# Kernel tuning notes

Measured on AMD Instinct MI355X. Metric: run time of the kernel, lower is better.

The kernel has to match this reference:

```python
import jax, jax.numpy as jnp
import numpy as np

B, T, D = 2, 2048, 2048
H, HKV, HD = 16, 4, 128
I = 5632
EPS = 1e-5


def setup_inputs() -> dict:
    ks = jax.random.split(jax.random.key(0), 12)
    s = 0.02
    return {
        "x": jax.random.normal(ks[0], (B, T, D), jnp.float32),
        "rope_cos": jax.random.uniform(ks[1], (T, HD // 2), jnp.float32),
        "rope_sin": jax.random.uniform(ks[2], (T, HD // 2), jnp.float32),
        "ln1_w": jnp.ones((D,), jnp.float32),
        "ln2_w": jnp.ones((D,), jnp.float32),
        "wq_w": jax.random.normal(ks[3], (D, H * HD), jnp.float32) * s,
        "wq_b": jnp.zeros((H * HD,), jnp.float32),
        "wk_w": jax.random.normal(ks[4], (D, HKV * HD), jnp.float32) * s,
        "wk_b": jnp.zeros((HKV * HD,), jnp.float32),
        "wv_w": jax.random.normal(ks[5], (D, HKV * HD), jnp.float32) * s,
        "wv_b": jnp.zeros((HKV * HD,), jnp.float32),
        "wo_w": jax.random.normal(ks[6], (H * HD, D), jnp.float32) * s,
        "wo_b": jnp.zeros((D,), jnp.float32),
        "w1_w": jax.random.normal(ks[7], (D, 2 * I), jnp.float32) * s,
        "w1_b": jnp.zeros((2 * I,), jnp.float32),
        "w2_w": jax.random.normal(ks[8], (I, D), jnp.float32) * s,
        "w2_b": jnp.zeros((D,), jnp.float32),
    }


def _rmsnorm(x, w):
    return x * jax.lax.rsqrt(jnp.mean(x * x, axis=-1, keepdims=True) + EPS) * w


def _rotate(x, cos, sin):
    # x: [B, h, T, HD]; cos/sin: [T, HD/2] broadcast over [B, h, T, HD/2]
    x1, x2 = x[..., ::2], x[..., 1::2]
    return jnp.stack([x1 * cos - x2 * sin, x1 * sin + x2 * cos], axis=-1).reshape(x.shape)


def reference(x, rope_cos, rope_sin, ln1_w, ln2_w, wq_w, wq_b, wk_w, wk_b,
              wv_w, wv_b, wo_w, wo_b, w1_w, w1_b, w2_w, w2_b):
    h = _rmsnorm(x, ln1_w)
    q = (h @ wq_w + wq_b).reshape(B, T, H, HD).transpose(0, 2, 1, 3)
    k = (h @ wk_w + wk_b).reshape(B, T, HKV, HD).transpose(0, 2, 1, 3)
    v = (h @ wv_w + wv_b).reshape(B, T, HKV, HD).transpose(0, 2, 1, 3)
    q = _rotate(q, rope_cos, rope_sin)
    k = _rotate(k, rope_cos, rope_sin)
    rep = H // HKV
    k = jnp.repeat(k, rep, axis=1)  # GQA repeat_interleave over head dim
    v = jnp.repeat(v, rep, axis=1)
    scale = 1.0 / np.sqrt(HD).astype(np.float32)
    scores = jnp.einsum('bhqd,bhkd->bhqk', q, k) * scale  # [B,H,T,T]
    causal = jnp.tril(jnp.ones((T, T), bool))
    scores = jnp.where(causal, scores, -jnp.inf)
    attn = jax.nn.softmax(scores, axis=-1)
    out = jnp.einsum('bhqk,bhkd->bhqd', attn, v)
    out = out.transpose(0, 2, 1, 3).reshape(B, T, H * HD) @ wo_w + wo_b
    h1 = x + out
    g = _rmsnorm(h1, ln2_w)
    gate_up = g @ w1_w + w1_b
    gate, up = gate_up[..., :I], gate_up[..., I:]
    mlp = (jax.nn.silu(gate) * up) @ w2_w + w2_b
    return h1 + mlp
```

## Files before the change

### kernel.cpp

```cpp
#include <hip/hip_runtime.h>

#define T_SEQ 2048
#define DMODEL 2048
#define NH 16
#define NKV 4
#define HD 128
#define ISZ 5632
#define BATCH 2
#define QKS 2560
#define QKVN 3072

typedef unsigned short ushort_t;
typedef __attribute__((ext_vector_type(8))) short short8;
typedef __attribute__((ext_vector_type(4))) float f32x4;

__device__ __forceinline__ ushort_t f2bf(float f) {
  unsigned int u = __float_as_uint(f);
  unsigned int r = (u + 0x7FFFu + ((u >> 16) & 1u)) >> 16;
  return (ushort_t)r;
}
__device__ __forceinline__ float bf2f(ushort_t h) {
  return __uint_as_float(((unsigned int)h) << 16);
}

__global__ __launch_bounds__(256) void wconv_kernel(const float* __restrict__ W,
                                                    ushort_t* __restrict__ Wt,
                                                    int K, int N) {
  __shared__ float tile[32][33];
  const int n0 = blockIdx.x * 32, k0 = blockIdx.y * 32;
  const int t = threadIdx.x;
  const int r = t >> 3, c = (t & 7) * 4;
  float4 v = *(const float4*)(W + (size_t)(k0 + r) * N + n0 + c);
  tile[r][c + 0] = v.x; tile[r][c + 1] = v.y; tile[r][c + 2] = v.z; tile[r][c + 3] = v.w;
  __syncthreads();
  ushort4 o;
  o.x = f2bf(tile[c + 0][r]);
  o.y = f2bf(tile[c + 1][r]);
  o.z = f2bf(tile[c + 2][r]);
  o.w = f2bf(tile[c + 3][r]);
  *(ushort4*)(Wt + (size_t)(n0 + r) * K + k0 + c) = o;
}

__global__ __launch_bounds__(256) void catbias_kernel(const float* __restrict__ a,
                                                      const float* __restrict__ b,
                                                      const float* __restrict__ c,
                                                      float* __restrict__ o) {
  int i = blockIdx.x * 256 + threadIdx.x;
  if (i < QKVN) o[i] = (i < 2048) ? a[i] : (i < QKS) ? b[i - 2048] : c[i - QKS];
}

__global__ __launch_bounds__(256) void rmsnorm_kernel(const float* __restrict__ x,
                                                      const float* __restrict__ w,
                                                      ushort_t* __restrict__ out) {
  const int row = blockIdx.x;
  const int t = threadIdx.x;
  const float* xr = x + (size_t)row * DMODEL;
  float4 v0 = *(const float4*)(xr + t * 4);
  float4 v1 = *(const float4*)(xr + 1024 + t * 4);
  float ss = v0.x * v0.x + v0.y * v0.y + v0.z * v0.z + v0.w * v0.w +
             v1.x * v1.x + v1.y * v1.y + v1.z * v1.z + v1.w * v1.w;
  #pragma unroll
  for (int m = 1; m < 64; m <<= 1) ss += __shfl_xor(ss, m);
  __shared__ float red[4];
  if ((t & 63) == 0) red[t >> 6] = ss;
  __syncthreads();
  float tot = red[0] + red[1] + red[2] + red[3];
  float rinv = rsqrtf(tot * (1.0f / DMODEL) + 1e-5f);
  float4 w0 = *(const float4*)(w + t * 4);
  float4 w1 = *(const float4*)(w + 1024 + t * 4);
  ushort4 o0, o1;
  o0.x = f2bf(v0.x * rinv * w0.x); o0.y = f2bf(v0.y * rinv * w0.y);
  o0.z = f2bf(v0.z * rinv * w0.z); o0.w = f2bf(v0.w * rinv * w0.w);
  o1.x = f2bf(v1.x * rinv * w1.x); o1.y = f2bf(v1.y * rinv * w1.y);
  o1.z = f2bf(v1.z * rinv * w1.z); o1.w = f2bf(v1.w * rinv * w1.w);
  *(ushort4*)(out + (size_t)row * DMODEL + t * 4) = o0;
  *(ushort4*)(out + (size_t)row * DMODEL + 1024 + t * 4) = o1;
}

__global__ __launch_bounds__(256) void swiglu_kernel(ushort_t* __restrict__ gu) {
  size_t i = (size_t)blockIdx.x * 256 + threadIdx.x;
  size_t m = i / (ISZ / 8);
  size_t j = (i % (ISZ / 8)) * 8;
  ushort_t* pg = gu + m * (2 * ISZ) + j;
  short8 gg = *(const short8*)pg;
  short8 uu = *(const short8*)(pg + ISZ);
  short8 oo;
  #pragma unroll
  for (int q = 0; q < 8; ++q) {
    float gv = bf2f((ushort_t)gg[q]);
    float uv = bf2f((ushort_t)uu[q]);
    float sl = gv / (1.f + __expf(-gv));
    oo[q] = (short)f2bf(sl * uv);
  }
  *(short8*)pg = oo;
}

template <int MODE>
__global__ __launch_bounds__(512, 2)
void gemm256_kernel(const ushort_t* __restrict__ A, int lda,
                    const ushort_t* __restrict__ Bt,
                    const float* __restrict__ bias, void* __restrict__ outp,
                    int M, int N, int K,
                    const float* __restrict__ rc, const float* __restrict__ rs,
                    ushort_t* __restrict__ outp2) {
  __shared__ ushort_t lds[65536];
  const int tid = threadIdx.x;
  const int wid = tid >> 6, lane = tid & 63;
  const int lq = lane & 15, g = lane >> 4;
  const int wm = wid >> 2, wn = wid & 3;
  const int m0 = blockIdx.x * 256, n0 = blockIdx.y * 256;
  const int NT = K >> 6;

  const char* ldsc = (const char*)lds;
  const int c0 = ((g ^ (lq & 3)) << 4) | (((lq >> 2) & 1) << 6);
  const int rbA = wm * 8192 + lq * 128 + c0;
  const int rbAx = rbA ^ 64;
  const int rbB = 32768 + wn * 4096 + lq * 128 + c0;
  const int rbBx = rbB ^ 64;

  const int l3 = lane >> 3;
  const int clog = ((lane & 7) ^ l3) << 4;
  const int s0 = wid * 16 + l3, s1 = s0 + 8;
  const int rA0 = (s0 & 63) + ((s0 >> 6) << 7);
  const int rA0b = (s1 & 63) + ((s1 >> 6) << 7);
  const int rB0 = ((s0 >> 5) << 6) + (s0 & 31);
  const int rB0b = ((s1 >> 5) << 6) + (s1 & 31);
  const char* pA0a = (const char*)A + (size_t)(m0 + rA0) * (lda * 2) + clog;
  const char* pA0b = (const char*)A + (size_t)(m0 + rA0b) * (lda * 2) + clog;
  const char* pA1a = pA0a + (size_t)64 * (lda * 2);
  const char* pA1b = pA0b + (size_t)64 * (lda * 2);
  const char* pB0a = (const char*)Bt + (size_t)(n0 + rB0) * (K * 2) + clog;
  const char* pB0b = (const char*)Bt + (size_t)(n0 + rB0b) * (K * 2) + clog;
  const char* pB1a = pB0a + (size_t)32 * (K * 2);
  const char* pB1b = pB0b + (size_t)32 * (K * 2);
  ushort_t* sd = lds + wid * 1024;

#define GLL(SRC, DOFF)                                                        \
  __builtin_amdgcn_global_load_lds(                                           \
      (const __attribute__((address_space(1))) void*)(SRC),                   \
      (__attribute__((address_space(3))) void*)(sd + (DOFF)), 16, 0, 0)
#define STG_ALL(PB)                                                           \
  {                                                                           \
    GLL(pA0a, (PB)*32768 + 0);     GLL(pA0b, (PB)*32768 + 512);               \
    GLL(pB0a, (PB)*32768 + 16384); GLL(pB0b, (PB)*32768 + 16896);             \
    GLL(pB1a, (PB)*32768 + 24576); GLL(pB1b, (PB)*32768 + 25088);             \
    GLL(pA1a, (PB)*32768 + 8192);  GLL(pA1b, (PB)*32768 + 8704);              \
    pA0a += 128; pA0b += 128; pA1a += 128; pA1b += 128;                       \
    pB0a += 128; pB0b += 128; pB1a += 128; pB1b += 128;                       \
  }

  f32x4 acc[8][4] = {};

#define TILE(P, DOST)                                                         \
  {                                                                           \
    asm volatile("s_waitcnt vmcnt(0)" ::: "memory");                          \
    __builtin_amdgcn_s_barrier();                                             \
    if (DOST) STG_ALL((P) ^ 1)                                                \
    short8 aA0[4][2], aA1[4][2], bb0[2][2], bb1[2][2];                        \
    _Pragma("unroll") for (int mi = 0; mi < 4; ++mi) {                        \
      aA0[mi][0] = *(const short8*)(ldsc + (P)*65536 + rbA + mi * 2048);      \
      aA0[mi][1] = *(const short8*)(ldsc + (P)*65536 + rbAx + mi * 2048);     \
    }                                                                         \
    _Pragma("unroll") for (int nj = 0; nj < 2; ++nj) {                        \
      bb0[nj][0] = *(const short8*)(ldsc + (P)*65536 + rbB + nj * 2048);      \
      bb0[nj][1] = *(const short8*)(ldsc + (P)*65536 + rbBx + nj * 2048);     \
    }                                                                         \
    _Pragma("unroll") for (int mi = 0; mi < 4; ++mi)                          \
      _Pragma("unroll") for (int nj = 0; nj < 2; ++nj) {                      \
        acc[mi][nj] = __builtin_amdgcn_mfma_f32_16x16x32_bf16(aA0[mi][0], bb0[nj][0], acc[mi][nj], 0, 0, 0); \
        acc[mi][nj] = __builtin_amdgcn_mfma_f32_16x16x32_bf16(aA0[mi][1], bb0[nj][1], acc[mi][nj], 0, 0, 0); \
      }                                                                       \
    _Pragma("unroll") for (int nj = 0; nj < 2; ++nj) {                        \
      bb1[nj][0] = *(const short8*)(ldsc + (P)*65536 + rbB + 16384 + nj * 2048);  \
      bb1[nj][1] = *(const short8*)(ldsc + (P)*65536 + rbBx + 16384 + nj * 2048); \
    }                                                                         \
    _Pragma("unroll") for (int mi = 0; mi < 4; ++mi)                          \
      _Pragma("unroll") for (int nj = 0; nj < 2; ++nj) {                      \
        acc[mi][2 + nj] = __builtin_amdgcn_mfma_f32_16x16x32_bf16(aA0[mi][0], bb1[nj][0], acc[mi][2 + nj], 0, 0, 0); \
        acc[mi][2 + nj] = __builtin_amdgcn_mfma_f32_16x16x32_bf16(aA0[mi][1], bb1[nj][1], acc[mi][2 + nj], 0, 0, 0); \
      }                                                                       \
    _Pragma("unroll") for (int mi = 0; mi < 4; ++mi) {                        \
      aA1[mi][0] = *(const short8*)(ldsc + (P)*65536 + rbA + 16384 + mi * 2048);  \
      aA1[mi][1] = *(const short8*)(ldsc + (P)*65536 + rbAx + 16384 + mi * 2048); \
    }                                                                         \
    _Pragma("unroll") for (int mi = 0; mi < 4; ++mi)                          \
      _Pragma("unroll") for (int nj = 0; nj < 2; ++nj) {                      \
        acc[4 + mi][nj] = __builtin_amdgcn_mfma_f32_16x16x32_bf16(aA1[mi][0], bb0[nj][0], acc[4 + mi][nj], 0, 0, 0); \
        acc[4 + mi][nj] = __builtin_amdgcn_mfma_f32_16x16x32_bf16(aA1[mi][1], bb0[nj][1], acc[4 + mi][nj], 0, 0, 0); \
      }                                                                       \
    _Pragma("unroll") for (int mi = 0; mi < 4; ++mi)                          \
      _Pragma("unroll") for (int nj = 0; nj < 2; ++nj) {                      \
        acc[4 + mi][2 + nj] = __builtin_amdgcn_mfma_f32_16x16x32_bf16(aA1[mi][0], bb1[nj][0], acc[4 + mi][2 + nj], 0, 0, 0); \
        acc[4 + mi][2 + nj] = __builtin_amdgcn_mfma_f32_16x16x32_bf16(aA1[mi][1], bb1[nj][1], acc[4 + mi][2 + nj], 0, 0, 0); \
      }                                                                       \
  }

  STG_ALL(0)
  for (int it = 0; it + 2 < NT; it += 2) {
    TILE(0, true)
    TILE(1, true)
  }
  TILE(0, true)
  TILE(1, false)
#undef TILE
#undef GLL
#undef STG_ALL

  #pragma unroll
  for (int nf = 0; nf < 4; ++nf) {
    int c = n0 + wn * 64 + nf * 16 + lq;
    float bb = bias[c];
    int d = (c & (HD - 1)) >> 1;
    #pragma unroll
    for (int mf = 0; mf < 8; ++mf) {
      #pragma unroll
      for (int i = 0; i < 4; ++i) {
        int r = m0 + wm * 128 + mf * 16 + g * 4 + i;
        float av = acc[mf][nf][i] + bb;
        if (MODE == 2) {
          if (c < QKS) {
            float pr = __shfl_xor(av, 1);
            int t = r & (T_SEQ - 1);
            float co = rc[t * 64 + d];
            float si = rs[t * 64 + d];
            float ov = (lq & 1) ? (pr * si + av * co) : (av * co - pr * si);
            ((ushort_t*)outp)[(size_t)r * QKS + c] = f2bf(ov);
          } else {
            int cv = c - QKS;
            int hk = cv >> 7, dd = cv & (HD - 1);
            int b2 = r >> 11, t2 = r & (T_SEQ - 1);
            outp2[((size_t)(b2 * NKV + hk) * HD + dd) * T_SEQ + t2] = f2bf(av);
          }
        } else {
          ((ushort_t*)outp)[(size_t)r * N + c] = f2bf(av);
        }
      }
    }
  }
}

__global__ __launch_bounds__(512, 1)
void gemm128_kernel(const ushort_t* __restrict__ A, int lda,
                    const ushort_t* __restrict__ Bt,
                    const float* __restrict__ bias, const float* __restrict__ res,
                    float* __restrict__ outp, int M, int N, int K) {
  __shared__ ushort_t lds[49152];
  const int tid = threadIdx.x;
  const int wid = tid >> 6, lane = tid & 63;
  const int lq = lane & 15, g = lane >> 4;
  const int wm = wid & 1, wn = wid >> 1;
  const int m0 = blockIdx.x * 128, n0 = blockIdx.y * 256;
  const int NT = K >> 6;

  const char* ldsc = (const char*)lds;
  const int c0 = ((g ^ (lq & 3)) << 4) | (((lq >> 2) & 1) << 6);
  const int rbA = wm * 8192 + lq * 128 + c0;
  const int rbAx = rbA ^ 64;
  const int rbB = 16384 + wn * 8192 + lq * 128 + c0;
  const int rbBx = rbB ^ 64;

  const char* pA[2];
  const char* pB[4];
  #pragma unroll
  for (int j = 0; j < 2; ++j) {
    int pb = (wid * 2 + j) * 1024 + lane * 16;
    int ob = pb ^ (((pb >> 7) & 7) << 4);
    pA[j] = (const char*)A + (size_t)(m0 + (ob >> 7)) * (lda * 2) + (ob & 127);
  }
  #pragma unroll
  for (int j = 0; j < 4; ++j) {
    int pb = (wid * 4 + j) * 1024 + lane * 16;
    int ob = pb ^ (((pb >> 7) & 7) << 4);
    pB[j] = (const char*)Bt + (size_t)(n0 + (ob >> 7)) * (K * 2) + (ob & 127);
  }
  ushort_t* sdA = lds + wid * 1024;
  ushort_t* sdB = lds + 8192 + wid * 2048;

#define GLL1(SRC, DST)                                                        \
  __builtin_amdgcn_global_load_lds(                                           \
      (const __attribute__((address_space(1))) void*)(SRC),                   \
      (__attribute__((address_space(3))) void*)(DST), 16, 0, 0)
#define STG128(PB)                                                            \
  {                                                                           \
    GLL1(pA[0], sdA + (PB)*24576 + 0);   GLL1(pA[1], sdA + (PB)*24576 + 512); \
    GLL1(pB[0], sdB + (PB)*24576 + 0);   GLL1(pB[1], sdB + (PB)*24576 + 512); \
    GLL1(pB[2], sdB + (PB)*24576 + 1024); GLL1(pB[3], sdB + (PB)*24576 + 1536); \
    pA[0] += 128; pA[1] += 128;                                               \
    pB[0] += 128; pB[1] += 128; pB[2] += 128; pB[3] += 128;                   \
  }

  f32x4 acc[4][4] = {};

#define TILE128(P, TCUR)                                                      \
  {                                                                           \
    asm volatile("s_waitcnt vmcnt(0)" ::: "memory");                          \
    __builtin_amdgcn_s_barrier();                                             \
    if ((TCUR) + 1 < NT) STG128((P) ^ 1)                                      \
    short8 aA[4][2], bb[4][2];                                                \
    _Pragma("unroll") for (int mi = 0; mi < 4; ++mi) {                        \
      aA[mi][0] = *(const short8*)(ldsc + (P)*49152 + rbA + mi * 2048);       \
      aA[mi][1] = *(const short8*)(ldsc + (P)*49152 + rbAx + mi * 2048);      \
    }                                                                         \
    _Pragma("unroll") for (int nj = 0; nj < 4; ++nj) {                        \
      bb[nj][0] = *(const short8*)(ldsc + (P)*49152 + rbB + nj * 2048);       \
      bb[nj][1] = *(const short8*)(ldsc + (P)*49152 + rbBx + nj * 2048);      \
    }                                                                         \
    _Pragma("unroll") for (int mi = 0; mi < 4; ++mi)                          \
      _Pragma("unroll") for (int nj = 0; nj < 4; ++nj) {                      \
        acc[mi][nj] = __builtin_amdgcn_mfma_f32_16x16x32_bf16(aA[mi][0], bb[nj][0], acc[mi][nj], 0, 0, 0); \
        acc[mi][nj] = __builtin_amdgcn_mfma_f32_16x16x32_bf16(aA[mi][1], bb[nj][1], acc[mi][nj], 0, 0, 0); \
      }                                                                       \
  }

  STG128(0)
  for (int t = 0; t < NT; t += 2) {
    TILE128(0, t)
    TILE128(1, t + 1)
  }
#undef TILE128
#undef GLL1
#undef STG128

  #pragma unroll
  for (int nf = 0; nf < 4; ++nf) {
    int c = n0 + wn * 64 + nf * 16 + lq;
    float bb = bias[c];
    #pragma unroll
    for (int mf = 0; mf < 4; ++mf) {
      #pragma unroll
      for (int i = 0; i < 4; ++i) {
        int r = m0 + wm * 64 + mf * 16 + g * 4 + i;
        size_t oidx = (size_t)r * N + c;
        outp[oidx] = res[oidx] + acc[mf][nf][i] + bb;
      }
    }
  }
}

#define QB 128
#define KB 64
#define PSTR 72

__global__ __launch_bounds__(256, 2)
void attn_kernel(const ushort_t* __restrict__ qk, const ushort_t* __restrict__ vT,
                 ushort_t* __restrict__ ao) {
  __shared__ ushort_t Klds[KB * 128];
  __shared__ ushort_t Vlds[HD * 64];
  __shared__ ushort_t Plds[4][16 * PSTR];

  const int tid = threadIdx.x;
  const int w = tid >> 6, lane = tid & 63;
  const int lq = lane & 15, g = lane >> 4;
  const int nqb = T_SEQ / QB;
  const int xq = blockIdx.x;
  const int qi = (xq & 1) ? (nqb - 1 - (xq >> 1)) : (xq >> 1);
  const int qb = qi * QB;
  const int h = blockIdx.y;
  const int b = blockIdx.z;
  const int hkv = h >> 2;
  const float scale = 0.08838834764831845f;

  short8 qf[2][4];
  #pragma unroll
  for (int gi = 0; gi < 2; ++gi) {
    const ushort_t* qrow = qk + ((size_t)(b * T_SEQ + qb + gi * 64 + w * 16 + lq) * QKS) + h * HD;
    #pragma unroll
    for (int ks = 0; ks < 4; ++ks) qf[gi][ks] = *(const short8*)(qrow + ks * 32 + g * 8);
  }

  f32x4 of[2][8] = {};
  float m_run[2] = {-1e30f, -1e30f};
  float l_run[2] = {0.f, 0.f};

  const char* kbaseC = (const char*)(qk + (size_t)b * T_SEQ * QKS + 2048 + hkv * HD);
  const char* vbaseC = (const char*)(vT + (size_t)(b * NKV + hkv) * HD * T_SEQ);
  const char* pK[4];
  const char* pV[4];
  #pragma unroll
  for (int j = 0; j < 4; ++j) {
    int krow = w * 16 + j * 4 + (lane >> 4);
    int kcol = ((lane & 15) * 16) ^ ((krow & 7) << 4);
    pK[j] = kbaseC + (size_t)krow * (QKS * 2) + kcol;
    int vrow = w * 32 + j * 8 + (lane >> 3);
    int vcol = ((lane & 7) * 16) ^ ((vrow & 7) << 4);
    pV[j] = vbaseC + (size_t)vrow * (T_SEQ * 2) + vcol;
  }
  ushort_t* kdst = Klds + w * 2048;
  ushort_t* vdst = Vlds + w * 2048;
  const char* kldsC = (const char*)Klds;
  const char* vldsC = (const char*)Vlds;

#define AGLL(SRC, DST)                                                        \
  __builtin_amdgcn_global_load_lds(                                           \
      (const __attribute__((address_space(1))) void*)(SRC),                   \
      (__attribute__((address_space(3))) void*)(DST), 16, 0, 0)

  const int nt = qb / KB + 2;
  for (int ti = 0; ti < nt; ++ti) {
    const int kt = ti * KB;
    #pragma unroll
    for (int j = 0; j < 4; ++j) {
      AGLL(pK[j], kdst + j * 512);
      AGLL(pV[j], vdst + j * 512);
      pK[j] += (size_t)KB * (QKS * 2);
      pV[j] += KB * 2;
    }
    asm volatile("s_waitcnt vmcnt(0)" ::: "memory");
    __builtin_amdgcn_s_barrier();

    #pragma unroll
    for (int gi = 0; gi < 2; ++gi) {
      const int qw = qb + gi * 64 + w * 16;
      if (kt <= qw + 15) {
        f32x4 s[4] = {};
        __builtin_amdgcn_s_setprio(1);
        #pragma unroll
        for (int c = 0; c < 4; ++c) {
          int krow = c * 16 + lq;
          #pragma unroll
          for (int ks = 0; ks < 4; ++ks) {
            short8 kf = *(const short8*)(kldsC + krow * 256 + (((ks * 64) + g * 16) ^ ((krow & 7) << 4)));
            s[c] = __builtin_amdgcn_mfma_f32_16x16x32_bf16(kf, qf[gi][ks], s[c], 0, 0, 0);
          }
        }
        __builtin_amdgcn_s_setprio(0);
        const int qg = qw + lq;
        float sv[16];
        #pragma unroll
        for (int c = 0; c < 4; ++c)
          #pragma unroll
          for (int i = 0; i < 4; ++i) {
            int kvg = kt + c * 16 + 4 * g + i;
            float xx = s[c][i] * scale;
            sv[c * 4 + i] = (kvg > qg) ? -1e30f : xx;
          }
        float tmax = sv[0];
        #pragma unroll
        for (int j = 1; j < 16; ++j) tmax = fmaxf(tmax, sv[j]);
        tmax = fmaxf(tmax, __shfl_xor(tmax, 16));
        tmax = fmaxf(tmax, __shfl_xor(tmax, 32));
        float mnew = fmaxf(m_run[gi], tmax);
        float corr = __expf(m_run[gi] - mnew);
        float pv[16];
        float ps = 0.f;
        #pragma unroll
        for (int j = 0; j < 16; ++j) { pv[j] = __expf(sv[j] - mnew); ps += pv[j]; }
        ps += __shfl_xor(ps, 16);
        ps += __shfl_xor(ps, 32);
        l_run[gi] = l_run[gi] * corr + ps;
        m_run[gi] = mnew;
        float c4[4];
        #pragma unroll
        for (int i = 0; i < 4; ++i) c4[i] = __shfl(corr, 4 * g + i);
        #pragma unroll
        for (int n = 0; n < 8; ++n)
          #pragma unroll
          for (int i = 0; i < 4; ++i) of[gi][n][i] *= c4[i];
        #pragma unroll
        for (int c = 0; c < 4; ++c) {
          ushort4 pw;
          pw.x = f2bf(pv[c * 4 + 0]); pw.y = f2bf(pv[c * 4 + 1]);
          pw.z = f2bf(pv[c * 4 + 2]); pw.w = f2bf(pv[c * 4 + 3]);
          *(ushort4*)(&Plds[w][lq * PSTR + c * 16 + 4 * g]) = pw;
        }
        short8 pf0 = *(const short8*)(&Plds[w][lq * PSTR + g * 8]);
        short8 pf1 = *(const short8*)(&Plds[w][lq * PSTR + 32 + g * 8]);
        __builtin_amdgcn_s_setprio(1);
        #pragma unroll
        for (int n = 0; n < 8; ++n) {
          int vr = n * 16 + lq;
          short8 vf0 = *(const short8*)(vldsC + vr * 128 + ((g * 16) ^ ((vr & 7) << 4)));
          short8 vf1 = *(const short8*)(vldsC + vr * 128 + ((64 + g * 16) ^ ((vr & 7) << 4)));
          of[gi][n] = __builtin_amdgcn_mfma_f32_16x16x32_bf16(pf0, vf0, of[gi][n], 0, 0, 0);
          of[gi][n] = __builtin_amdgcn_mfma_f32_16x16x32_bf16(pf1, vf1, of[gi][n], 0, 0, 0);
        }
        __builtin_amdgcn_s_setprio(0);
      }
    }
    __builtin_amdgcn_s_barrier();
  }
#undef AGLL

  #pragma unroll
  for (int gi = 0; gi < 2; ++gi) {
    float li[4];
    #pragma unroll
    for (int i = 0; i < 4; ++i) li[i] = 1.f / __shfl(l_run[gi], 4 * g + i);
    #pragma unroll
    for (int n = 0; n < 8; ++n)
      #pragma unroll
      for (int i = 0; i < 4; ++i) {
        int tok = qb + gi * 64 + w * 16 + 4 * g + i;
        ao[((size_t)(b * T_SEQ + tok) * (NH * HD)) + h * HD + n * 16 + lq] = f2bf(of[gi][n][i] * li[i]);
      }
  }
}

extern "C" void kernel_launch(void* const* d_in, const int* in_sizes, int n_in,
                              void* d_out, int out_size, void* d_ws, size_t ws_size,
                              hipStream_t stream) {
  const float* x   = (const float*)d_in[0];
  const float* rc  = (const float*)d_in[1];
  const float* rs  = (const float*)d_in[2];
  const float* ln1 = (const float*)d_in[3];
  const float* ln2 = (const float*)d_in[4];
  const float* wq  = (const float*)d_in[5];
  const float* wqb = (const float*)d_in[6];
  const float* wk  = (const float*)d_in[7];
  const float* wkb = (const float*)d_in[8];
  const float* wv  = (const float*)d_in[9];
  const float* wvb = (const float*)d_in[10];
  const float* wo  = (const float*)d_in[11];
  const float* wob = (const float*)d_in[12];
  const float* w1  = (const float*)d_in[13];
  const float* w1b = (const float*)d_in[14];
  const float* w2  = (const float*)d_in[15];
  const float* w2b = (const float*)d_in[16];

  char* ws = (char*)d_ws;
  size_t off = 0;
  auto alloc = [&](size_t bytes) {
    char* p = ws + off;
    off += (bytes + 255) & ~(size_t)255;
    return (void*)p;
  };
  const int M = BATCH * T_SEQ;
  ushort_t* w1T  = (ushort_t*)alloc((size_t)11264 * 2048 * 2);
  ushort_t* w2T  = (ushort_t*)alloc((size_t)2048 * 5632 * 2);
  ushort_t* hbuf = (ushort_t*)alloc((size_t)M * 2048 * 2);
  ushort_t* vbufT= (ushort_t*)alloc((size_t)M * 512 * 2);
  float*    qkvb = (float*)alloc((size_t)QKVN * 4);
  size_t guStart = off;
  ushort_t* wqkvT = (ushort_t*)alloc((size_t)QKVN * 2048 * 2);
  ushort_t* woT  = (ushort_t*)alloc((size_t)2048 * 2048 * 2);
  ushort_t* qkbuf= (ushort_t*)alloc((size_t)M * QKS * 2);
  size_t guBytes = (size_t)M * 11264 * 2;
  size_t used = off - guStart;
  if (guBytes > used) alloc(guBytes - used);
  ushort_t* gu = (ushort_t*)(ws + guStart);
  float* h1 = (float*)d_out;
  if (off > ws_size) return;

  wconv_kernel<<<dim3(2048 / 32, 2048 / 32), 256, 0, stream>>>(wq, wqkvT, 2048, 2048);
  wconv_kernel<<<dim3(512 / 32, 2048 / 32), 256, 0, stream>>>(wk, wqkvT + (size_t)2048 * 2048, 2048, 512);
  wconv_kernel<<<dim3(512 / 32, 2048 / 32), 256, 0, stream>>>(wv, wqkvT + (size_t)QKS * 2048, 2048, 512);
  wconv_kernel<<<dim3(2048 / 32, 2048 / 32), 256, 0, stream>>>(wo, woT, 2048, 2048);
  wconv_kernel<<<dim3(11264 / 32, 2048 / 32), 256, 0, stream>>>(w1, w1T, 2048, 11264);
  wconv_kernel<<<dim3(2048 / 32, 5632 / 32), 256, 0, stream>>>(w2, w2T, 5632, 2048);
  catbias_kernel<<<12, 256, 0, stream>>>(wqb, wkb, wvb, qkvb);

  rmsnorm_kernel<<<M, 256, 0, stream>>>(x, ln1, hbuf);

  gemm256_kernel<2><<<dim3(M / 256, QKVN / 256), 512, 0, stream>>>(
      hbuf, 2048, wqkvT, qkvb, qkbuf, M, QKVN, 2048, rc, rs, vbufT);

  attn_kernel<<<dim3(T_SEQ / QB, NH, BATCH), 256, 0, stream>>>(qkbuf, vbufT, hbuf);

  gemm128_kernel<<<dim3(M / 128, 2048 / 256), 512, 0, stream>>>(hbuf, 2048, woT, wob, x, h1, M, 2048, 2048);

  rmsnorm_kernel<<<M, 256, 0, stream>>>(h1, ln2, hbuf);

  gemm256_kernel<0><<<dim3(M / 256, 11264 / 256), 512, 0, stream>>>(
      hbuf, 2048, w1T, w1b, gu, M, 11264, 2048, nullptr, nullptr, nullptr);

  swiglu_kernel<<<(M * (ISZ / 8)) / 256, 256, 0, stream>>>(gu);

  gemm128_kernel<<<dim3(M / 128, 2048 / 256), 512, 0, stream>>>(gu, 11264, w2T, w2b, h1, (float*)d_out, M, 2048, 5632);

  (void)in_sizes; (void)n_in; (void)out_size;
}
```

Baseline: 631.5 us.

## Fuse SwiGLU into gate/up GEMM epilogue via interleaved W1 columns

The W1 transpose now interleaves gate and up columns in 16-wide groups, so each GEMM tile holds matching gate and up fragments. The GEMM epilogue (new MODE 3) applies bias and SiLU(gate)*up and writes only the M x ISZ activation, which removes the separate swiglu kernel and the full gate_up write and reread. The grid is also swapped so blockIdx.x walks N, which changes the order tiles are scheduled in and how weight and activation tiles are reused across blocks. The epilogue does more arithmetic and its stores are narrower and scattered.

```diff
diff --git a/kernel.cpp b/kernel.cpp
--- a/kernel.cpp
+++ b/kernel.cpp
@@ -41,6 +41,27 @@
   *(ushort4*)(Wt + (size_t)(n0 + r) * K + k0 + c) = o;
 }
 
+__global__ __launch_bounds__(256) void wconvP_kernel(const float* __restrict__ W,
+                                                     ushort_t* __restrict__ Wt,
+                                                     int K, int N) {
+  __shared__ float tile[32][33];
+  const int n0 = blockIdx.x * 32, k0 = blockIdx.y * 32;
+  const int t = threadIdx.x;
+  const int r = t >> 3, c = (t & 7) * 4;
+  float4 v = *(const float4*)(W + (size_t)(k0 + r) * N + n0 + c);
+  tile[r][c + 0] = v.x; tile[r][c + 1] = v.y; tile[r][c + 2] = v.z; tile[r][c + 3] = v.w;
+  __syncthreads();
+  ushort4 o;
+  o.x = f2bf(tile[c + 0][r]);
+  o.y = f2bf(tile[c + 1][r]);
+  o.z = f2bf(tile[c + 2][r]);
+  o.w = f2bf(tile[c + 3][r]);
+  int n = n0 + r;
+  int np = (n < ISZ) ? ((n >> 4) << 5) + (n & 15)
+                     : (((n - ISZ) >> 4) << 5) + 16 + ((n - ISZ) & 15);
+  *(ushort4*)(Wt + (size_t)np * K + k0 + c) = o;
+}
+
 __global__ __launch_bounds__(256) void catbias_kernel(const float* __restrict__ a,
                                                       const float* __restrict__ b,
                                                       const float* __restrict__ c,
@@ -77,24 +98,6 @@
   *(ushort4*)(out + (size_t)row * DMODEL + 1024 + t * 4) = o1;
 }
 
-__global__ __launch_bounds__(256) void swiglu_kernel(ushort_t* __restrict__ gu) {
-  size_t i = (size_t)blockIdx.x * 256 + threadIdx.x;
-  size_t m = i / (ISZ / 8);
-  size_t j = (i % (ISZ / 8)) * 8;
-  ushort_t* pg = gu + m * (2 * ISZ) + j;
-  short8 gg = *(const short8*)pg;
-  short8 uu = *(const short8*)(pg + ISZ);
-  short8 oo;
-  #pragma unroll
-  for (int q = 0; q < 8; ++q) {
-    float gv = bf2f((ushort_t)gg[q]);
-    float uv = bf2f((ushort_t)uu[q]);
-    float sl = gv / (1.f + __expf(-gv));
-    oo[q] = (short)f2bf(sl * uv);
-  }
-  *(short8*)pg = oo;
-}
-
 template <int MODE>
 __global__ __launch_bounds__(512, 2)
 void gemm256_kernel(const ushort_t* __restrict__ A, int lda,
@@ -108,7 +111,8 @@
   const int wid = tid >> 6, lane = tid & 63;
   const int lq = lane & 15, g = lane >> 4;
   const int wm = wid >> 2, wn = wid & 3;
-  const int m0 = blockIdx.x * 256, n0 = blockIdx.y * 256;
+  const int m0 = (MODE == 2 ? blockIdx.x : blockIdx.y) * 256;
+  const int n0 = (MODE == 2 ? blockIdx.y : blockIdx.x) * 256;
   const int NT = K >> 6;
 
   const char* ldsc = (const char*)lds;
@@ -206,33 +210,54 @@
 #undef GLL
 #undef STG_ALL
 
-  #pragma unroll
-  for (int nf = 0; nf < 4; ++nf) {
-    int c = n0 + wn * 64 + nf * 16 + lq;
-    float bb = bias[c];
-    int d = (c & (HD - 1)) >> 1;
-    #pragma unroll
-    for (int mf = 0; mf < 8; ++mf) {
+  if (MODE == 3) {
+    #pragma unroll
+    for (int nf = 0; nf < 4; nf += 2) {
+      int cg = n0 + wn * 64 + nf * 16 + lq;
+      int G = ((cg >> 5) << 4) | (cg & 15);
+      float bg = bias[G];
+      float bu = bias[ISZ + G];
       #pragma unroll
-      for (int i = 0; i < 4; ++i) {
-        int r = m0 + wm * 128 + mf * 16 + g * 4 + i;
-        float av = acc[mf][nf][i] + bb;
-        if (MODE == 2) {
-          if (c < QKS) {
-            float pr = __shfl_xor(av, 1);
-            int t = r & (T_SEQ - 1);
-            float co = rc[t * 64 + d];
-            float si = rs[t * 64 + d];
-            float ov = (lq & 1) ? (pr * si + av * co) : (av * co - pr * si);
-            ((ushort_t*)outp)[(size_t)r * QKS + c] = f2bf(ov);
+      for (int mf = 0; mf < 8; ++mf) {
+        #pragma unroll
+        for (int i = 0; i < 4; ++i) {
+          int r = m0 + wm * 128 + mf * 16 + g * 4 + i;
+          float gv = acc[mf][nf][i] + bg;
+          float uv = acc[mf][nf + 1][i] + bu;
+          float sl = gv / (1.f + __expf(-gv));
+          ((ushort_t*)outp)[(size_t)r * ISZ + G] = f2bf(sl * uv);
+        }
+      }
+    }
+  } else {
+    #pragma unroll
+    for (int nf = 0; nf < 4; ++nf) {
+      int c = n0 + wn * 64 + nf * 16 + lq;
+      float bb = bias[c];
+      int d = (c & (HD - 1)) >> 1;
+      #pragma unroll
+      for (int mf = 0; mf < 8; ++mf) {
+        #pragma unroll
+        for (int i = 0; i < 4; ++i) {
+          int r = m0 + wm * 128 + mf * 16 + g * 4 + i;
+          float av = acc[mf][nf][i] + bb;
+          if (MODE == 2) {
+            if (c < QKS) {
+              float pr = __shfl_xor(av, 1);
+              int t = r & (T_SEQ - 1);
+              float co = rc[t * 64 + d];
+              float si = rs[t * 64 + d];
+              float ov = (lq & 1) ? (pr * si + av * co) : (av * co - pr * si);
+              ((ushort_t*)outp)[(size_t)r * QKS + c] = f2bf(ov);
+            } else {
+              int cv = c - QKS;
+              int hk = cv >> 7, dd = cv & (HD - 1);
+              int b2 = r >> 11, t2 = r & (T_SEQ - 1);
+              outp2[((size_t)(b2 * NKV + hk) * HD + dd) * T_SEQ + t2] = f2bf(av);
+            }
           } else {
-            int cv = c - QKS;
-            int hk = cv >> 7, dd = cv & (HD - 1);
-            int b2 = r >> 11, t2 = r & (T_SEQ - 1);
-            outp2[((size_t)(b2 * NKV + hk) * HD + dd) * T_SEQ + t2] = f2bf(av);
+            ((ushort_t*)outp)[(size_t)r * N + c] = f2bf(av);
           }
-        } else {
-          ((ushort_t*)outp)[(size_t)r * N + c] = f2bf(av);
         }
       }
     }
@@ -534,10 +559,10 @@
   ushort_t* wqkvT = (ushort_t*)alloc((size_t)QKVN * 2048 * 2);
   ushort_t* woT  = (ushort_t*)alloc((size_t)2048 * 2048 * 2);
   ushort_t* qkbuf= (ushort_t*)alloc((size_t)M * QKS * 2);
-  size_t guBytes = (size_t)M * 11264 * 2;
+  size_t actBytes = (size_t)M * ISZ * 2;
   size_t used = off - guStart;
-  if (guBytes > used) alloc(guBytes - used);
-  ushort_t* gu = (ushort_t*)(ws + guStart);
+  if (actBytes > used) alloc(actBytes - used);
+  ushort_t* act = (ushort_t*)(ws + guStart);
   float* h1 = (float*)d_out;
   if (off > ws_size) return;
 
@@ -545,7 +570,7 @@
   wconv_kernel<<<dim3(512 / 32, 2048 / 32), 256, 0, stream>>>(wk, wqkvT + (size_t)2048 * 2048, 2048, 512);
   wconv_kernel<<<dim3(512 / 32, 2048 / 32), 256, 0, stream>>>(wv, wqkvT + (size_t)QKS * 2048, 2048, 512);
   wconv_kernel<<<dim3(2048 / 32, 2048 / 32), 256, 0, stream>>>(wo, woT, 2048, 2048);
-  wconv_kernel<<<dim3(11264 / 32, 2048 / 32), 256, 0, stream>>>(w1, w1T, 2048, 11264);
+  wconvP_kernel<<<dim3(11264 / 32, 2048 / 32), 256, 0, stream>>>(w1, w1T, 2048, 11264);
   wconv_kernel<<<dim3(2048 / 32, 5632 / 32), 256, 0, stream>>>(w2, w2T, 5632, 2048);
   catbias_kernel<<<12, 256, 0, stream>>>(wqb, wkb, wvb, qkvb);
 
@@ -560,12 +585,10 @@
 
   rmsnorm_kernel<<<M, 256, 0, stream>>>(h1, ln2, hbuf);
 
-  gemm256_kernel<0><<<dim3(M / 256, 11264 / 256), 512, 0, stream>>>(
-      hbuf, 2048, w1T, w1b, gu, M, 11264, 2048, nullptr, nullptr, nullptr);
-
-  swiglu_kernel<<<(M * (ISZ / 8)) / 256, 256, 0, stream>>>(gu);
-
-  gemm128_kernel<<<dim3(M / 128, 2048 / 256), 512, 0, stream>>>(gu, 11264, w2T, w2b, h1, (float*)d_out, M, 2048, 5632);
+  gemm256_kernel<3><<<dim3(11264 / 256, M / 256), 512, 0, stream>>>(
+      hbuf, 2048, w1T, w1b, act, M, 11264, 2048, nullptr, nullptr, nullptr);
+
+  gemm128_kernel<<<dim3(M / 128, 2048 / 256), 512, 0, stream>>>(act, 5632, w2T, w2b, h1, (float*)d_out, M, 2048, 5632);
 
   (void)in_sizes; (void)n_in; (void)out_size;
 }
```

Measured after the change: 592.0 us, median of 2. 1.07x faster.
